# Performance work log

Measured on AMD Instinct MI355X. Metric: run time of the kernel, lower is better.

The kernel has to match this reference:

```python
import jax, jax.numpy as jnp
import numpy as np

D = 768; DEPTH = 12; NH = 12; DH = 64; MLP = 3072; P = 16; IMG = 224; HF = 14; FD = 256
B = 2; NV = 4


def _ln(x, g, b):
    m = x.mean(-1, keepdims=True)
    v = ((x - m) ** 2).mean(-1, keepdims=True)
    return (x - m) * jax.lax.rsqrt(v + 1e-6) * g + b


def _vit(x, patch_w, patch_b, cls_tok, pos_emb, blocks, nf_g, nf_b):
    # x: [n,3,224,224] -> tokens [n,197,768] (timm vit_base_patch16_224 forward_features)
    n = x.shape[0]
    p = x.reshape(n, 3, HF, P, HF, P).transpose(0, 2, 4, 1, 3, 5).reshape(n, HF * HF, 3 * P * P)
    tok = p @ patch_w + patch_b
    tok = jnp.concatenate([jnp.broadcast_to(cls_tok, (n, 1, D)), tok], axis=1) + pos_emb

    def block(t, pr):
        l1g, l1b, qw, qb, pw, pb, l2g, l2b, f1w, f1b, f2w, f2b = pr
        h = _ln(t, l1g, l1b)
        qkv = (h @ qw + qb).reshape(n, -1, 3, NH, DH)
        q, k, v = qkv[:, :, 0], qkv[:, :, 1], qkv[:, :, 2]
        att = jax.nn.softmax(jnp.einsum('bqhd,bkhd->bhqk', q, k) / jnp.sqrt(jnp.float32(DH)), axis=-1)
        o = jnp.einsum('bhqk,bkhd->bqhd', att, v).reshape(n, -1, D)
        t = t + o @ pw + pb
        h = _ln(t, l2g, l2b)
        t = t + jax.nn.gelu(h @ f1w + f1b, approximate=False) @ f2w + f2b
        return t, None

    tok, _ = jax.lax.scan(block, tok, blocks)
    return _ln(tok, nf_g, nf_b)


def setup_inputs() -> dict:
    key = jax.random.key(0)
    ks = jax.random.split(key, 24)
    s = 0.02
    imgs = jax.random.normal(ks[0], (B, NV, 3, IMG, IMG), jnp.float32)
    depths = jax.random.uniform(ks[1], (B, NV, IMG, IMG), jnp.float32) * 0.05  # scaled *65.535 -> (0,3.3), inside (0,5)
    t = jax.random.normal(ks[2], (B, NV, 3), jnp.float32) * 0.5
    poses = jnp.broadcast_to(jnp.eye(4, dtype=jnp.float32), (B, NV, 4, 4)).at[:, :, :3, 3].set(t)
    intr = (jnp.zeros((B, NV, 3, 3), jnp.float32)
            .at[:, :, 0, 0].set(200.0).at[:, :, 1, 1].set(200.0)
            .at[:, :, 0, 2].set(112.0).at[:, :, 1, 2].set(112.0).at[:, :, 2, 2].set(1.0))
    grid_points = jax.random.normal(ks[3], (B, 196, 3), jnp.float32)
    d = dict(
        ugv_images=imgs, ugv_depths=depths, camera_poses=poses, intrinsics=intr,
        grid_points_3d=grid_points,
        patch_w=jax.random.normal(ks[4], (3 * P * P, D), jnp.float32) * s,
        patch_b=jnp.zeros((D,), jnp.float32),
        cls_tok=jax.random.normal(ks[5], (1, 1, D), jnp.float32) * s,
        pos_emb=jax.random.normal(ks[6], (1, HF * HF + 1, D), jnp.float32) * s,
        ln1_g=jnp.ones((DEPTH, D), jnp.float32), ln1_b=jnp.zeros((DEPTH, D), jnp.float32),
        qkv_w=jax.random.normal(ks[7], (DEPTH, D, 3 * D), jnp.float32) * s,
        qkv_b=jnp.zeros((DEPTH, 3 * D), jnp.float32),
        proj_w=jax.random.normal(ks[8], (DEPTH, D, D), jnp.float32) * s,
        proj_b=jnp.zeros((DEPTH, D), jnp.float32),
        ln2_g=jnp.ones((DEPTH, D), jnp.float32), ln2_b=jnp.zeros((DEPTH, D), jnp.float32),
        fc1_w=jax.random.normal(ks[9], (DEPTH, D, MLP), jnp.float32) * s,
        fc1_b=jnp.zeros((DEPTH, MLP), jnp.float32),
        fc2_w=jax.random.normal(ks[10], (DEPTH, MLP, D), jnp.float32) * s,
        fc2_b=jnp.zeros((DEPTH, D), jnp.float32),
        nf_g=jnp.ones((D,), jnp.float32), nf_b=jnp.zeros((D,), jnp.float32),
        conv_w=jax.random.normal(ks[11], (FD, D), jnp.float32) * s,
        conv_b=jnp.zeros((FD,), jnp.float32),
    )
    return d


def reference(ugv_images, ugv_depths, camera_poses, intrinsics, grid_points_3d,
              patch_w, patch_b, cls_tok, pos_emb,
              ln1_g, ln1_b, qkv_w, qkv_b, proj_w, proj_b,
              ln2_g, ln2_b, fc1_w, fc1_b, fc2_w, fc2_b,
              nf_g, nf_b, conv_w, conv_b):
    blocks = (ln1_g, ln1_b, qkv_w, qkv_b, proj_w, proj_b, ln2_g, ln2_b, fc1_w, fc1_b, fc2_w, fc2_b)
    tok = _vit(ugv_images.reshape(B * NV, 3, IMG, IMG), patch_w, patch_b, cls_tok, pos_emb, blocks, nf_g, nf_b)
    feats = tok[:, 1:, :].transpose(0, 2, 1).reshape(B, NV, D, HF, HF)  # [B,N,C,Hf,Wf]

    # swap rows 0,1 of w2c, then invert
    w2c = camera_poses[:, :, jnp.array([1, 0, 2, 3]), :]
    c2w = jnp.linalg.inv(w2c)

    d = jax.image.resize(ugv_depths, (B, NV, HF, HF), 'linear', antialias=False) * (65535.0 / 1000.0)
    mask = (d > 0.0) & (d < 5.0)

    fx = intrinsics[:, :, 0, 0][..., None, None]
    fy = intrinsics[:, :, 1, 1][..., None, None]
    cx = intrinsics[:, :, 0, 2][..., None, None]
    cy = intrinsics[:, :, 1, 2][..., None, None]

    u, v = jnp.meshgrid(jnp.arange(HF, dtype=jnp.float32), jnp.arange(HF, dtype=jnp.float32), indexing='xy')
    Xc = -((u - cx) * d / (fx + 1e-8))
    Yc = (v - cy) * d / (fy + 1e-8)
    pts = jnp.stack([Xc, Yc, d, jnp.ones_like(d)], axis=-1)  # [B,N,Hf,Wf,4]
    w = jnp.einsum('bnij,bnhwj->bnhwi', c2w, pts)
    Xw, Yw = w[..., 0], w[..., 1]

    tile = 10.0
    px = Xw * (HF / tile) + HF / 2.0
    py = -(Yw * (HF / tile)) + HF / 2.0
    pxi = jnp.round(px).astype(jnp.int32)
    pyi = jnp.round(py).astype(jnp.int32)
    inb = (pxi >= 0) & (pxi < HF) & (pyi >= 0) & (pyi < HF)
    valid = mask & inb

    HW = HF * HF
    boff = jnp.arange(B, dtype=jnp.int32)[:, None, None, None] * HW
    idx = jnp.where(valid, boff + pyi * HF + pxi, B * HW).reshape(-1)  # invalid -> dummy bucket
    src = feats.transpose(0, 1, 3, 4, 2).reshape(-1, D)  # [B*N*HW, C]
    seg = B * HW + 1

    ssum = jax.ops.segment_sum(src, idx, num_segments=seg)
    cnt = jax.ops.segment_sum(valid.astype(jnp.float32).reshape(-1), idx, num_segments=seg)
    smax = jnp.zeros((seg, D), src.dtype).at[idx].max(src)  # include_self with 0 init, like torch amax

    avg = ssum[:B * HW] / (cnt[:B * HW, None] + 1e-8)
    bev = (avg + smax[:B * HW]) / 2.0
    bev = bev.reshape(B, HF, HF, D)
    out = jnp.einsum('bhwc,oc->bohw', bev, conv_w) + conv_b[None, :, None, None]
    return out
```

## Files before the change

### kernel.cpp

```cpp
#include <hip/hip_runtime.h>
#include <hip/hip_bf16.h>
#include <math.h>
#include <type_traits>
#include <utility>

#define DMODEL 768
#define NTOK 197
#define NIMG 8
#define NHEADS 12
#define MLPD 3072
#define NROWS (NIMG*NTOK)
#define NPATCH (NIMG*196)
#define HF 14
#define BATCH 2
#define NCELL (BATCH*HF*HF)
#define FD 256

typedef __attribute__((ext_vector_type(8))) short s8v;
typedef __attribute__((ext_vector_type(8))) __bf16 b8v;
typedef __attribute__((ext_vector_type(8))) _Float16 h8v;
typedef __attribute__((ext_vector_type(4))) float f32x4;

template <typename V, typename = void>
struct mfma_takes : std::false_type {};
template <typename V>
struct mfma_takes<V, std::void_t<decltype(
    __builtin_amdgcn_mfma_f32_16x16x32_bf16(std::declval<V>(), std::declval<V>(),
                                            std::declval<f32x4>(), 0, 0, 0))>>
    : std::true_type {};

template <typename V>
struct MfmaCall {
    static __device__ inline f32x4 run(s8v a, s8v b, f32x4 c) {
        return __builtin_amdgcn_mfma_f32_16x16x32_bf16(
            __builtin_bit_cast(V, a), __builtin_bit_cast(V, b), c, 0, 0, 0);
    }
};
using mfma_v = std::conditional_t<mfma_takes<b8v>::value, b8v, s8v>;

template <typename V, typename = void>
struct mfma16_takes : std::false_type {};
template <typename V>
struct mfma16_takes<V, std::void_t<decltype(
    __builtin_amdgcn_mfma_f32_16x16x32_f16(std::declval<V>(), std::declval<V>(),
                                           std::declval<f32x4>(), 0, 0, 0))>>
    : std::true_type {};

template <typename V>
struct MfmaF16Call {
    static __device__ inline f32x4 run(s8v a, s8v b, f32x4 c) {
        return __builtin_amdgcn_mfma_f32_16x16x32_f16(
            __builtin_bit_cast(V, a), __builtin_bit_cast(V, b), c, 0, 0, 0);
    }
};
using mfma16_v = std::conditional_t<mfma16_takes<h8v>::value, h8v, s8v>;

typedef __attribute__((address_space(1))) const unsigned int guint_t;
typedef __attribute__((address_space(3))) unsigned int luint_t;

template <int BM, int BN>
__global__ __launch_bounds__(256) void gemm_t(
    const __hip_bfloat16* __restrict__ A, const __hip_bfloat16* __restrict__ BT,
    const float* __restrict__ bias, const float* __restrict__ res,
    void* __restrict__ Cout, int M, int N, int K, int flags, int nx,
    float* __restrict__ part)
{
    constexpr int FM = BM / 32;
    constexpr int FN = BN / 32;
    __shared__ short Asl[BM * 32];
    __shared__ short Bsl[BN * 32];
    int t = threadIdx.x;
    int w = t >> 6, lane = t & 63;

    int nwg = gridDim.x;
    int id = blockIdx.x;
    int q = nwg >> 3, r = nwg & 7;
    int xcd = id & 7;
    int wgid = (xcd < r ? xcd * (q + 1) : r * (q + 1) + (xcd - r) * q) + (id >> 3);
    int bx = wgid % nx, by = wgid / nx;
    int bm = by * BM, bn = bx * BN;

    int S = gridDim.z, z = blockIdx.z;
    int kchunk = K / S;
    int kbeg = z * kchunk, kend = kbeg + kchunk;

    int rbase = (w >> 1) * (BM / 2), cbase = (w & 1) * (BN / 2);

    f32x4 acc[FM][FN];
    #pragma unroll
    for (int i = 0; i < FM; i++)
        #pragma unroll
        for (int j = 0; j < FN; j++)
            acc[i][j] = (f32x4){0.f, 0.f, 0.f, 0.f};

    const short* Ag = (const short*)A;
    const short* Bg = (const short*)BT;

    for (int k0 = kbeg; k0 < kend; k0 += 32) {
        #pragma unroll
        for (int i = 0; i < BM * 4 / 256; i++) {
            int c = i * 256 + t;
            int row = c >> 2, koff = (c & 3) * 8;
            int ga = bm + row; if (ga >= M) ga = M - 1;
            __builtin_amdgcn_global_load_lds(
                (guint_t*)(Ag + (size_t)ga * K + k0 + koff),
                (luint_t*)(Asl + c * 8), 16, 0, 0);
        }
        #pragma unroll
        for (int i = 0; i < BN * 4 / 256; i++) {
            int c = i * 256 + t;
            int row = c >> 2, koff = (c & 3) * 8;
            __builtin_amdgcn_global_load_lds(
                (guint_t*)(Bg + (size_t)(bn + row) * K + k0 + koff),
                (luint_t*)(Bsl + c * 8), 16, 0, 0);
        }
        __syncthreads();

        int kk = (lane >> 4) * 8;
        int rl = lane & 15;
        s8v af[FM], bfr[FN];
        #pragma unroll
        for (int i = 0; i < FM; i++)
            af[i] = *(const s8v*)(Asl + (rbase + i * 16 + rl) * 32 + kk);
        #pragma unroll
        for (int j = 0; j < FN; j++)
            bfr[j] = *(const s8v*)(Bsl + (cbase + j * 16 + rl) * 32 + kk);
        #pragma unroll
        for (int i = 0; i < FM; i++)
            #pragma unroll
            for (int j = 0; j < FN; j++)
                acc[i][j] = MfmaCall<mfma_v>::run(af[i], bfr[j], acc[i][j]);
        __syncthreads();
    }

    int colg = lane & 15;
    int rowg = (lane >> 4) * 4;
    #pragma unroll
    for (int i = 0; i < FM; i++) {
        #pragma unroll
        for (int j = 0; j < FN; j++) {
            #pragma unroll
            for (int qq = 0; qq < 4; qq++) {
                int rr = bm + rbase + i * 16 + rowg + qq;
                int cc = bn + cbase + j * 16 + colg;
                if (rr < M) {
                    float v = acc[i][j][qq];
                    if (flags & 8) {
                        part[((size_t)z * M + rr) * N + cc] = v;
                    } else {
                        if (bias) v += bias[cc];
                        if (flags & 1) v = 0.5f * v * (1.0f + erff(v * 0.7071067811865476f));
                        if (res)  v += res[(size_t)rr * N + cc];
                        if (flags & 2)
                            ((__hip_bfloat16*)Cout)[(size_t)rr * N + cc] = __float2bfloat16(v);
                        else if (flags & 4)
                            ((_Float16*)Cout)[(size_t)rr * N + cc] = (_Float16)v;
                        else
                            ((float*)Cout)[(size_t)rr * N + cc] = v;
                    }
                }
            }
        }
    }
}

__global__ __launch_bounds__(256) void fc2_reduce(
    const float* __restrict__ part, const float* __restrict__ bias,
    float* __restrict__ tok)
{
    int i = blockIdx.x * 256 + threadIdx.x;
    if (i >= NROWS * DMODEL / 4) return;
    float4 p0 = ((const float4*)part)[i];
    float4 p1 = ((const float4*)(part + (size_t)NROWS * DMODEL))[i];
    float4 tv = ((float4*)tok)[i];
    int c = (i * 4) % DMODEL;
    float4 bv = *(const float4*)(bias + c);
    tv.x += p0.x + p1.x + bv.x;
    tv.y += p0.y + p1.y + bv.y;
    tv.z += p0.z + p1.z + bv.z;
    tv.w += p0.w + p1.w + bv.w;
    ((float4*)tok)[i] = tv;
}

#define AT_STR 232
#define KS_STR 72

__global__ __launch_bounds__(256) void fused_attn_kernel(
    const _Float16* __restrict__ qkv, __hip_bfloat16* __restrict__ O)
{
    __shared__ char smem[29696 + 59392];
    _Float16* Vt = (_Float16*)smem;
    _Float16* Qs = (_Float16*)(smem + 29696);
    _Float16* Ks = Qs + 128 * KS_STR;
    _Float16* Pl = (_Float16*)(smem + 29696);

    int nh = blockIdx.x;
    int n = nh / NHEADS, hh = nh % NHEADS;
    int qoff = blockIdx.y * 128;
    int t = threadIdx.x;
    int w = t >> 6, lane = t & 63;
    int g = lane >> 4, rl = lane & 15;
    const _Float16* base = qkv + (size_t)n * NTOK * 2304;

    for (int idx = t; idx < 208 * 8; idx += 256) {
        int row = idx >> 3, c8 = (idx & 7) * 8;
        if (row < NTOK)
            *(uint4*)(Ks + row * KS_STR + c8) =
                *(const uint4*)(base + (size_t)row * 2304 + 768 + hh * 64 + c8);
        else
            *(uint4*)(Ks + row * KS_STR + c8) = make_uint4(0, 0, 0, 0);
    }
    for (int idx = t; idx < 128 * 8; idx += 256) {
        int row = idx >> 3, c8 = (idx & 7) * 8;
        int gq = qoff + row; if (gq > NTOK - 1) gq = NTOK - 1;
        *(uint4*)(Qs + row * KS_STR + c8) =
            *(const uint4*)(base + (size_t)gq * 2304 + hh * 64 + c8);
    }
    for (int idx = t; idx < NTOK * 8; idx += 256) {
        int k = idx >> 3, dg = (idx & 7) * 8;
        _Float16 tmp[8];
        *(uint4*)tmp = *(const uint4*)(base + (size_t)k * 2304 + 1536 + hh * 64 + dg);
        #pragma unroll
        for (int j = 0; j < 8; j++) Vt[(dg + j) * AT_STR + k] = tmp[j];
    }
    for (int idx = t; idx < 64 * 27; idx += 256) {
        int d = idx / 27, k = NTOK + idx % 27;
        Vt[d * AT_STR + k] = (_Float16)0.f;
    }
    __syncthreads();

    int wq0 = w * 32;
    f32x4 sacc[2][13];
    #pragma unroll
    for (int i = 0; i < 2; i++)
        #pragma unroll
        for (int tt = 0; tt < 13; tt++)
            sacc[i][tt] = (f32x4){0.f, 0.f, 0.f, 0.f};

    #pragma unroll
    for (int s = 0; s < 2; s++) {
        s8v af[2];
        #pragma unroll
        for (int i = 0; i < 2; i++)
            af[i] = *(const s8v*)(Qs + (wq0 + i * 16 + rl) * KS_STR + s * 32 + 8 * g);
        #pragma unroll
        for (int tt = 0; tt < 13; tt++) {
            s8v bf = *(const s8v*)(Ks + (tt * 16 + rl) * KS_STR + s * 32 + 8 * g);
            #pragma unroll
            for (int i = 0; i < 2; i++)
                sacc[i][tt] = MfmaF16Call<mfma16_v>::run(af[i], bf, sacc[i][tt]);
        }
    }
    __syncthreads();

    _Float16* Pw = Pl + w * 32 * AT_STR;
    #pragma unroll
    for (int i = 0; i < 2; i++) {
        #pragma unroll
        for (int r = 0; r < 4; r++) {
            float vv[13];
            float mx = -3.0e38f;
            #pragma unroll
            for (int tt = 0; tt < 13; tt++) {
                float v = sacc[i][tt][r] * 0.125f;
                vv[tt] = v;
                if (rl + 16 * tt < NTOK) mx = fmaxf(mx, v);
            }
            mx = fmaxf(mx, __shfl_xor(mx, 1));
            mx = fmaxf(mx, __shfl_xor(mx, 2));
            mx = fmaxf(mx, __shfl_xor(mx, 4));
            mx = fmaxf(mx, __shfl_xor(mx, 8));
            float pv[13];
            float sum = 0.f;
            #pragma unroll
            for (int tt = 0; tt < 13; tt++) {
                float p = (rl + 16 * tt < NTOK) ? __expf(vv[tt] - mx) : 0.f;
                pv[tt] = p; sum += p;
            }
            sum += __shfl_xor(sum, 1);
            sum += __shfl_xor(sum, 2);
            sum += __shfl_xor(sum, 4);
            sum += __shfl_xor(sum, 8);
            float rinv = 1.0f / sum;
            int prow = i * 16 + g * 4 + r;
            #pragma unroll
            for (int tt = 0; tt < 13; tt++)
                Pw[prow * AT_STR + rl + 16 * tt] = (_Float16)(pv[tt] * rinv);
        }
    }
    for (int idx = lane; idx < 32 * 16; idx += 64) {
        int rr = idx >> 4, cc = 208 + (idx & 15);
        Pw[rr * AT_STR + cc] = (_Float16)0.f;
    }

    f32x4 oacc[2][4];
    #pragma unroll
    for (int i = 0; i < 2; i++)
        #pragma unroll
        for (int j = 0; j < 4; j++)
            oacc[i][j] = (f32x4){0.f, 0.f, 0.f, 0.f};

    for (int s = 0; s < 7; s++) {
        s8v pf[2], vf[4];
        #pragma unroll
        for (int i = 0; i < 2; i++)
            pf[i] = *(const s8v*)(Pw + (i * 16 + rl) * AT_STR + s * 32 + 8 * g);
        #pragma unroll
        for (int j = 0; j < 4; j++)
            vf[j] = *(const s8v*)(Vt + (j * 16 + rl) * AT_STR + s * 32 + 8 * g);
        #pragma unroll
        for (int i = 0; i < 2; i++)
            #pragma unroll
            for (int j = 0; j < 4; j++)
                oacc[i][j] = MfmaF16Call<mfma16_v>::run(pf[i], vf[j], oacc[i][j]);
    }

    #pragma unroll
    for (int i = 0; i < 2; i++) {
        #pragma unroll
        for (int j = 0; j < 4; j++) {
            #pragma unroll
            for (int r = 0; r < 4; r++) {
                int qidx = qoff + wq0 + i * 16 + g * 4 + r;
                if (qidx < NTOK) {
                    int d = j * 16 + rl;
                    O[((size_t)n * NTOK + qidx) * DMODEL + hh * 64 + d] =
                        __float2bfloat16(oacc[i][j][r]);
                }
            }
        }
    }
}

__device__ inline void transpose_tile(const float* __restrict__ src,
                                      __hip_bfloat16* __restrict__ dst,
                                      int K, int N, int b)
{
    __shared__ float tl[32][33];
    int nt = N >> 5;
    int n0 = (b % nt) * 32, k0 = (b / nt) * 32;
    int tx = threadIdx.x & 31, ty = threadIdx.x >> 5;
    #pragma unroll
    for (int i = 0; i < 4; i++)
        tl[ty + i * 8][tx] = src[(size_t)(k0 + ty + i * 8) * N + n0 + tx];
    __syncthreads();
    #pragma unroll
    for (int i = 0; i < 4; i++)
        dst[(size_t)(n0 + ty + i * 8) * K + k0 + tx] = __float2bfloat16(tl[tx][ty + i * 8]);
}

__global__ __launch_bounds__(256) void convT(const float* __restrict__ src,
                                             __hip_bfloat16* __restrict__ dst,
                                             int K, int N)
{
    transpose_tile(src, dst, K, N, blockIdx.x);
}

__global__ __launch_bounds__(256) void convT4(
    const float* __restrict__ s0, const float* __restrict__ s1,
    const float* __restrict__ s2, const float* __restrict__ s3,
    __hip_bfloat16* __restrict__ d0, __hip_bfloat16* __restrict__ d1,
    __hip_bfloat16* __restrict__ d2, __hip_bfloat16* __restrict__ d3)
{
    int b = blockIdx.x;
    const float* src; __hip_bfloat16* dst; int K, N;
    if (b < 1728)      {            src = s0; dst = d0; K = 768;  N = 2304; }
    else if (b < 2304) { b -= 1728; src = s1; dst = d1; K = 768;  N = 768;  }
    else if (b < 4608) { b -= 2304; src = s2; dst = d2; K = 768;  N = 3072; }
    else               { b -= 4608; src = s3; dst = d3; K = 3072; N = 768;  }
    transpose_tile(src, dst, K, N, b);
}

__global__ __launch_bounds__(256) void patch_extract_kernel(
    const float* __restrict__ img, __hip_bfloat16* __restrict__ Pm)
{
    size_t e = (size_t)blockIdx.x * 256 + threadIdx.x;
    if (e >= (size_t)NPATCH * DMODEL) return;
    int cidx = (int)(e % DMODEL);
    int r    = (int)(e / DMODEL);
    int n  = r / 196, s = r % 196;
    int hi = s / HF, wi = s % HF;
    int c  = cidx >> 8, py = (cidx >> 4) & 15, px = cidx & 15;
    Pm[e] = __float2bfloat16(
        img[(((size_t)n * 3 + c) * 224 + hi * 16 + py) * 224 + wi * 16 + px]);
}

__global__ __launch_bounds__(256) void assemble_tok_kernel(
    const float* __restrict__ tmp, const float* __restrict__ cls,
    const float* __restrict__ pos, float* __restrict__ tok)
{
    size_t e = (size_t)blockIdx.x * 256 + threadIdx.x;
    if (e >= (size_t)NROWS * DMODEL) return;
    int d = (int)(e % DMODEL);
    size_t rr = e / DMODEL;
    int n = (int)(rr / NTOK), r = (int)(rr % NTOK);
    float v = (r == 0) ? cls[d] : tmp[((size_t)n * 196 + r - 1) * DMODEL + d];
    tok[e] = v + pos[(size_t)r * DMODEL + d];
}

template <int OUT_BF16>
__global__ __launch_bounds__(256) void ln_kernel(
    const float* __restrict__ X, const float* __restrict__ g,
    const float* __restrict__ b, void* __restrict__ Yv)
{
    int r = blockIdx.x;
    int t = threadIdx.x;
    const float* x = X + (size_t)r * DMODEL;
    float v0 = x[t], v1 = x[t + 256], v2 = x[t + 512];
    __shared__ float red[8];
    float s = v0 + v1 + v2;
    #pragma unroll
    for (int m = 32; m >= 1; m >>= 1) s += __shfl_xor(s, m);
    int wid = t >> 6, lane = t & 63;
    if (lane == 0) red[wid] = s;
    __syncthreads();
    float mean = (red[0] + red[1] + red[2] + red[3]) * (1.0f / DMODEL);
    float d0 = v0 - mean, d1 = v1 - mean, d2 = v2 - mean;
    float q = d0 * d0 + d1 * d1 + d2 * d2;
    #pragma unroll
    for (int m = 32; m >= 1; m >>= 1) q += __shfl_xor(q, m);
    __syncthreads();
    if (lane == 0) red[4 + wid] = q;
    __syncthreads();
    float var = (red[4] + red[5] + red[6] + red[7]) * (1.0f / DMODEL);
    float rs = 1.0f / sqrtf(var + 1e-6f);
    float y0 = d0 * rs * g[t] + b[t];
    float y1 = d1 * rs * g[t + 256] + b[t + 256];
    float y2 = d2 * rs * g[t + 512] + b[t + 512];
    if (OUT_BF16) {
        __hip_bfloat16* y = (__hip_bfloat16*)Yv + (size_t)r * DMODEL;
        y[t] = __float2bfloat16(y0);
        y[t + 256] = __float2bfloat16(y1);
        y[t + 512] = __float2bfloat16(y2);
    } else {
        float* y = (float*)Yv + (size_t)r * DMODEL;
        y[t] = y0; y[t + 256] = y1; y[t + 512] = y2;
    }
}

__device__ void invert4(const float m[16], float out[16]) {
    float inv[16];
    inv[0] = m[5]*m[10]*m[15] - m[5]*m[11]*m[14] - m[9]*m[6]*m[15] + m[9]*m[7]*m[14] + m[13]*m[6]*m[11] - m[13]*m[7]*m[10];
    inv[4] = -m[4]*m[10]*m[15] + m[4]*m[11]*m[14] + m[8]*m[6]*m[15] - m[8]*m[7]*m[14] - m[12]*m[6]*m[11] + m[12]*m[7]*m[10];
    inv[8] = m[4]*m[9]*m[15] - m[4]*m[11]*m[13] - m[8]*m[5]*m[15] + m[8]*m[7]*m[13] + m[12]*m[5]*m[11] - m[12]*m[7]*m[9];
    inv[12] = -m[4]*m[9]*m[14] + m[4]*m[10]*m[13] + m[8]*m[5]*m[14] - m[8]*m[6]*m[13] - m[12]*m[5]*m[10] + m[12]*m[6]*m[9];
    inv[1] = -m[1]*m[10]*m[15] + m[1]*m[11]*m[14] + m[9]*m[2]*m[15] - m[9]*m[3]*m[14] - m[13]*m[2]*m[11] + m[13]*m[3]*m[10];
    inv[5] = m[0]*m[10]*m[15] - m[0]*m[11]*m[14] - m[8]*m[2]*m[15] + m[8]*m[3]*m[14] + m[12]*m[2]*m[11] - m[12]*m[3]*m[10];
    inv[9] = -m[0]*m[9]*m[15] + m[0]*m[11]*m[13] + m[8]*m[1]*m[15] - m[8]*m[3]*m[13] - m[12]*m[1]*m[11] + m[12]*m[3]*m[9];
    inv[13] = m[0]*m[9]*m[14] - m[0]*m[10]*m[13] - m[8]*m[1]*m[14] + m[8]*m[2]*m[13] + m[12]*m[1]*m[10] - m[12]*m[2]*m[9];
    inv[2] = m[1]*m[6]*m[15] - m[1]*m[7]*m[14] - m[5]*m[2]*m[15] + m[5]*m[3]*m[14] + m[13]*m[2]*m[7] - m[13]*m[3]*m[6];
    inv[6] = -m[0]*m[6]*m[15] + m[0]*m[7]*m[14] + m[4]*m[2]*m[15] - m[4]*m[3]*m[14] - m[12]*m[2]*m[7] + m[12]*m[3]*m[6];
    inv[10] = m[0]*m[5]*m[15] - m[0]*m[7]*m[13] - m[4]*m[1]*m[15] + m[4]*m[3]*m[13] + m[12]*m[1]*m[7] - m[12]*m[3]*m[5];
    inv[14] = -m[0]*m[5]*m[14] + m[0]*m[6]*m[13] + m[4]*m[1]*m[14] - m[4]*m[2]*m[13] - m[12]*m[1]*m[6] + m[12]*m[2]*m[5];
    inv[3] = -m[1]*m[6]*m[11] + m[1]*m[7]*m[10] + m[5]*m[2]*m[11] - m[5]*m[3]*m[10] - m[9]*m[2]*m[7] + m[9]*m[3]*m[6];
    inv[7] = m[0]*m[6]*m[11] - m[0]*m[7]*m[10] - m[4]*m[2]*m[11] + m[4]*m[3]*m[10] + m[8]*m[2]*m[7] - m[8]*m[3]*m[6];
    inv[11] = -m[0]*m[5]*m[11] + m[0]*m[7]*m[9] + m[4]*m[1]*m[11] - m[4]*m[3]*m[9] - m[8]*m[1]*m[7] + m[8]*m[3]*m[5];
    inv[15] = m[0]*m[5]*m[10] - m[0]*m[6]*m[9] - m[4]*m[1]*m[10] + m[4]*m[2]*m[9] + m[8]*m[1]*m[6] - m[8]*m[2]*m[5];
    float det = m[0]*inv[0] + m[1]*inv[4] + m[2]*inv[8] + m[3]*inv[12];
    det = 1.0f / det;
    for (int i = 0; i < 16; i++) out[i] = inv[i] * det;
}

__global__ __launch_bounds__(256) void bev_index_kernel(
    const float* __restrict__ depths, const float* __restrict__ poses,
    const float* __restrict__ intr, int* __restrict__ idxbuf)
{
    int bv = blockIdx.x;
    int b  = bv / 4;
    __shared__ float c2w[16];
    if (threadIdx.x == 0) {
        float w2c[16];
        const float* Pm = poses + bv * 16;
        const int perm[4] = {1, 0, 2, 3};
        for (int i = 0; i < 4; i++)
            for (int j = 0; j < 4; j++)
                w2c[i * 4 + j] = Pm[perm[i] * 4 + j];
        invert4(w2c, c2w);
    }
    __syncthreads();
    int t = threadIdx.x;
    if (t >= 196) return;
    int hh = t / HF, ww = t % HF;
    const float* dp = depths + (size_t)bv * 224 * 224;
    int r0 = hh * 16 + 7, c0 = ww * 16 + 7;
    float d = 0.25f * (dp[r0 * 224 + c0] + dp[r0 * 224 + c0 + 1] +
                       dp[(r0 + 1) * 224 + c0] + dp[(r0 + 1) * 224 + c0 + 1]);
    d *= 65.535f;
    bool mask = (d > 0.0f) && (d < 5.0f);
    float fx = intr[bv * 9 + 0], fy = intr[bv * 9 + 4];
    float cx = intr[bv * 9 + 2], cy = intr[bv * 9 + 5];
    float u = (float)ww, v = (float)hh;
    float Xc = -((u - cx) * d / (fx + 1e-8f));
    float Yc = (v - cy) * d / (fy + 1e-8f);
    float Xw = c2w[0] * Xc + c2w[1] * Yc + c2w[2] * d + c2w[3];
    float Yw = c2w[4] * Xc + c2w[5] * Yc + c2w[6] * d + c2w[7];
    float px = Xw * 1.4f + 7.0f;
    float py = -(Yw * 1.4f) + 7.0f;
    int pxi = (int)rintf(px);
    int pyi = (int)rintf(py);
    bool inb = (pxi >= 0) && (pxi < HF) && (pyi >= 0) && (pyi < HF);
    idxbuf[bv * 196 + t] = (mask && inb) ? (b * 196 + pyi * HF + pxi) : -1;
}

__global__ __launch_bounds__(256) void splat_kernel(
    const float* __restrict__ src, const int* __restrict__ idxbuf,
    float* __restrict__ ssum, float* __restrict__ smax, float* __restrict__ cnt)
{
    int r = blockIdx.x;
    int idx = idxbuf[r];
    if (idx < 0) return;
    int bv = r / 196, s = r % 196;
    const float* row = src + ((size_t)bv * NTOK + 1 + s) * DMODEL;
    int t = threadIdx.x;
    for (int d = t; d < DMODEL; d += 256) {
        float v = row[d];
        atomicAdd(&ssum[(size_t)idx * DMODEL + d], v);
        atomicMax((int*)(smax + (size_t)idx * DMODEL + d), __float_as_int(v));
    }
    if (t == 0) atomicAdd(&cnt[idx], 1.0f);
}

__global__ __launch_bounds__(256) void bev_conv_kernel(
    const float* __restrict__ ssum, const float* __restrict__ smax,
    const float* __restrict__ cnt, const float* __restrict__ convw,
    const float* __restrict__ convb, float* __restrict__ out)
{
    int cell = blockIdx.x;
    __shared__ float bev[DMODEL];
    int t = threadIdx.x;
    float c = cnt[cell];
    for (int d = t; d < DMODEL; d += 256)
        bev[d] = 0.5f * (ssum[(size_t)cell * DMODEL + d] / (c + 1e-8f) +
                         smax[(size_t)cell * DMODEL + d]);
    __syncthreads();
    float acc = convb[t];
    const float4* wr = (const float4*)(convw + (size_t)t * DMODEL);
    #pragma unroll 4
    for (int dc = 0; dc < DMODEL / 4; dc++) {
        float4 w4 = wr[dc];
        acc += bev[dc * 4 + 0] * w4.x + bev[dc * 4 + 1] * w4.y +
               bev[dc * 4 + 2] * w4.z + bev[dc * 4 + 3] * w4.w;
    }
    int b = cell / 196, s = cell % 196;
    out[((size_t)b * FD + t) * 196 + s] = acc;
}

extern "C" void kernel_launch(void* const* d_in, const int* in_sizes, int n_in,
                              void* d_out, int out_size, void* d_ws, size_t ws_size,
                              hipStream_t stream) {
    const float* imgs    = (const float*)d_in[0];
    const float* depths  = (const float*)d_in[1];
    const float* poses   = (const float*)d_in[2];
    const float* intr    = (const float*)d_in[3];
    const float* patch_w = (const float*)d_in[5];
    const float* patch_b = (const float*)d_in[6];
    const float* cls_tok = (const float*)d_in[7];
    const float* pos_emb = (const float*)d_in[8];
    const float* ln1_g   = (const float*)d_in[9];
    const float* ln1_b   = (const float*)d_in[10];
    const float* qkv_w   = (const float*)d_in[11];
    const float* qkv_b   = (const float*)d_in[12];
    const float* proj_w  = (const float*)d_in[13];
    const float* proj_b  = (const float*)d_in[14];
    const float* ln2_g   = (const float*)d_in[15];
    const float* ln2_b   = (const float*)d_in[16];
    const float* fc1_w   = (const float*)d_in[17];
    const float* fc1_b   = (const float*)d_in[18];
    const float* fc2_w   = (const float*)d_in[19];
    const float* fc2_b   = (const float*)d_in[20];
    const float* nf_g    = (const float*)d_in[21];
    const float* nf_b    = (const float*)d_in[22];
    const float* conv_w  = (const float*)d_in[23];
    const float* conv_b  = (const float*)d_in[24];
    float* out = (float*)d_out;
    float* ws  = (float*)d_ws;

    const size_t OFF_TOK  = 0;
    const size_t OFF_FB   = OFF_TOK + 1210368;
    const size_t OFF_PB   = OFF_FB  + 3631104;
    const size_t OFF_HB   = OFF_PB  + 3725664;
    const size_t OFF_WQ   = OFF_HB  + 605184;
    const size_t OFF_WP   = OFF_WQ  + 884736;
    const size_t OFF_WF1  = OFF_WP  + 294912;
    const size_t OFF_WF2  = OFF_WF1 + 1179648;
    const size_t OFF_SSUM = OFF_WF2 + 1179648;
    const size_t OFF_SMAX = OFF_SSUM + 301056;
    const size_t OFF_CNT  = OFF_SMAX + 301056;
    const size_t OFF_IDX  = OFF_CNT + 512;

    float* tok  = ws + OFF_TOK;
    float* fbig = ws + OFF_FB;
    float* pbuf = ws + OFF_PB;
    _Float16* qkv_h = (_Float16*)pbuf;
    __hip_bfloat16* hb  = (__hip_bfloat16*)(ws + OFF_HB);
    __hip_bfloat16* wq  = (__hip_bfloat16*)(ws + OFF_WQ);
    __hip_bfloat16* wp  = (__hip_bfloat16*)(ws + OFF_WP);
    __hip_bfloat16* wf1 = (__hip_bfloat16*)(ws + OFF_WF1);
    __hip_bfloat16* wf2 = (__hip_bfloat16*)(ws + OFF_WF2);
    float* ssum = ws + OFF_SSUM;
    float* smax = ws + OFF_SMAX;
    float* cnt  = ws + OFF_CNT;
    int*   idxb = (int*)(ws + OFF_IDX);

    const int MT = (NROWS + 63) / 64;
    const int MTP = (NPATCH + 63) / 64;

    convT<<<576, 256, 0, stream>>>(patch_w, wq, 768, 768);
    patch_extract_kernel<<<(NPATCH * DMODEL) / 256, 256, 0, stream>>>(imgs, hb);
    gemm_t<64, 64><<<dim3(12 * MTP, 1, 1), 256, 0, stream>>>(
        hb, wq, patch_b, nullptr, fbig, NPATCH, 768, 768, 0, 12, nullptr);
    assemble_tok_kernel<<<(NROWS * DMODEL) / 256, 256, 0, stream>>>(
        fbig, cls_tok, pos_emb, tok);

    for (int l = 0; l < 12; l++) {
        convT4<<<6912, 256, 0, stream>>>(
            qkv_w + (size_t)l * DMODEL * 2304, proj_w + (size_t)l * DMODEL * DMODEL,
            fc1_w + (size_t)l * DMODEL * MLPD, fc2_w + (size_t)l * MLPD * DMODEL,
            wq, wp, wf1, wf2);
        ln_kernel<1><<<NROWS, 256, 0, stream>>>(tok, ln1_g + l * DMODEL, ln1_b + l * DMODEL, hb);
        gemm_t<64, 128><<<dim3(18 * MT, 1, 1), 256, 0, stream>>>(
            hb, wq, qkv_b + (size_t)l * 2304, nullptr, qkv_h, NROWS, 2304, 768,
            4 , 18, nullptr);
        fused_attn_kernel<<<dim3(NIMG * NHEADS, 2), 256, 0, stream>>>(qkv_h, hb);
        gemm_t<64, 64><<<dim3(12 * MT, 1, 1), 256, 0, stream>>>(
            hb, wp, proj_b + (size_t)l * DMODEL, tok, tok, NROWS, 768, 768,
            0, 12, nullptr);
        ln_kernel<1><<<NROWS, 256, 0, stream>>>(tok, ln2_g + l * DMODEL, ln2_b + l * DMODEL, hb);
        gemm_t<64, 128><<<dim3(24 * MT, 1, 1), 256, 0, stream>>>(
            hb, wf1, fc1_b + (size_t)l * MLPD, nullptr, pbuf, NROWS, 3072, 768,
            3 , 24, nullptr);
        gemm_t<64, 64><<<dim3(12 * MT, 1, 2), 256, 0, stream>>>(
            (__hip_bfloat16*)pbuf, wf2, nullptr, nullptr, nullptr, NROWS, 768, 3072,
            8 , 12, fbig);
        fc2_reduce<<<(NROWS * DMODEL / 4 + 255) / 256, 256, 0, stream>>>(
            fbig, fc2_b + (size_t)l * DMODEL, tok);
    }

    ln_kernel<0><<<NROWS, 256, 0, stream>>>(tok, nf_g, nf_b, fbig);

    bev_index_kernel<<<NIMG, 256, 0, stream>>>(depths, poses, intr, idxb);
    hipMemsetAsync(ssum, 0, (2 * (size_t)NCELL * DMODEL + 512) * sizeof(float), stream);
    splat_kernel<<<NPATCH, 256, 0, stream>>>(fbig, idxb, ssum, smax, cnt);

    bev_conv_kernel<<<NCELL, 256, 0, stream>>>(ssum, smax, cnt, conv_w, conv_b, out);
}
```

Baseline: 1.736 ms.

## Fuse residual-reduce with LayerNorm, batch weight transposes, shrink attention query tile

Residual adds (proj and fc2 split-K partials plus bias) are fused with the following LayerNorm into one row kernel, and token assembly is fused with the first LN. This removes separate elementwise and LN passes over the token buffer. All layer weight transposes run in a single up-front launch into a larger workspace instead of one launch per layer. The attention kernel now uses 64-query tiles (one 16-row strip per wave) with four y-blocks instead of two, for more blocks and fewer registers per wave. The cost is a larger workspace and the proj GEMM now writing fp32 partials that are re-read by the reduce kernel.

```diff
diff --git a/kernel.cpp b/kernel.cpp
--- a/kernel.cpp
+++ b/kernel.cpp
@@ -164,22 +164,93 @@
     }
 }
 
-__global__ __launch_bounds__(256) void fc2_reduce(
+template <int NPART, int FINAL>
+__global__ __launch_bounds__(256) void redln_kernel(
     const float* __restrict__ part, const float* __restrict__ bias,
-    float* __restrict__ tok)
-{
-    int i = blockIdx.x * 256 + threadIdx.x;
-    if (i >= NROWS * DMODEL / 4) return;
-    float4 p0 = ((const float4*)part)[i];
-    float4 p1 = ((const float4*)(part + (size_t)NROWS * DMODEL))[i];
-    float4 tv = ((float4*)tok)[i];
-    int c = (i * 4) % DMODEL;
-    float4 bv = *(const float4*)(bias + c);
-    tv.x += p0.x + p1.x + bv.x;
-    tv.y += p0.y + p1.y + bv.y;
-    tv.z += p0.z + p1.z + bv.z;
-    tv.w += p0.w + p1.w + bv.w;
-    ((float4*)tok)[i] = tv;
+    float* __restrict__ tok, const float* __restrict__ g,
+    const float* __restrict__ b, __hip_bfloat16* __restrict__ hout,
+    float* __restrict__ fout)
+{
+    int r = blockIdx.x, t = threadIdx.x;
+    __shared__ float red[8];
+    float v[3];
+    #pragma unroll
+    for (int i = 0; i < 3; i++) {
+        int idx = t + i * 256;
+        float x = tok[(size_t)r * DMODEL + idx] + bias[idx];
+        x += part[(size_t)r * DMODEL + idx];
+        if (NPART == 2) x += part[((size_t)NROWS + r) * DMODEL + idx];
+        v[i] = x;
+        if (!FINAL) tok[(size_t)r * DMODEL + idx] = x;
+    }
+    float s = v[0] + v[1] + v[2];
+    #pragma unroll
+    for (int m = 32; m >= 1; m >>= 1) s += __shfl_xor(s, m);
+    int wid = t >> 6, lane = t & 63;
+    if (lane == 0) red[wid] = s;
+    __syncthreads();
+    float mean = (red[0] + red[1] + red[2] + red[3]) * (1.0f / DMODEL);
+    float d0 = v[0] - mean, d1 = v[1] - mean, d2 = v[2] - mean;
+    float qv = d0 * d0 + d1 * d1 + d2 * d2;
+    #pragma unroll
+    for (int m = 32; m >= 1; m >>= 1) qv += __shfl_xor(qv, m);
+    __syncthreads();
+    if (lane == 0) red[4 + wid] = qv;
+    __syncthreads();
+    float var = (red[4] + red[5] + red[6] + red[7]) * (1.0f / DMODEL);
+    float rs = 1.0f / sqrtf(var + 1e-6f);
+    float dd[3] = {d0, d1, d2};
+    #pragma unroll
+    for (int i = 0; i < 3; i++) {
+        int idx = t + i * 256;
+        float y = dd[i] * rs * g[idx] + b[idx];
+        if (FINAL) fout[(size_t)r * DMODEL + idx] = y;
+        else       hout[(size_t)r * DMODEL + idx] = __float2bfloat16(y);
+    }
+}
+
+__global__ __launch_bounds__(256) void assemble_ln_kernel(
+    const float* __restrict__ tmp, const float* __restrict__ cls,
+    const float* __restrict__ pos, const float* __restrict__ g,
+    const float* __restrict__ b, float* __restrict__ tok,
+    __hip_bfloat16* __restrict__ hout)
+{
+    int rr = blockIdx.x;
+    int n = rr / NTOK, r = rr % NTOK;
+    int t = threadIdx.x;
+    __shared__ float red[8];
+    float v[3];
+    #pragma unroll
+    for (int i = 0; i < 3; i++) {
+        int idx = t + i * 256;
+        float x = (r == 0) ? cls[idx]
+                           : tmp[((size_t)n * 196 + r - 1) * DMODEL + idx];
+        x += pos[(size_t)r * DMODEL + idx];
+        v[i] = x;
+        tok[(size_t)rr * DMODEL + idx] = x;
+    }
+    float s = v[0] + v[1] + v[2];
+    #pragma unroll
+    for (int m = 32; m >= 1; m >>= 1) s += __shfl_xor(s, m);
+    int wid = t >> 6, lane = t & 63;
+    if (lane == 0) red[wid] = s;
+    __syncthreads();
+    float mean = (red[0] + red[1] + red[2] + red[3]) * (1.0f / DMODEL);
+    float d0 = v[0] - mean, d1 = v[1] - mean, d2 = v[2] - mean;
+    float qv = d0 * d0 + d1 * d1 + d2 * d2;
+    #pragma unroll
+    for (int m = 32; m >= 1; m >>= 1) qv += __shfl_xor(qv, m);
+    __syncthreads();
+    if (lane == 0) red[4 + wid] = qv;
+    __syncthreads();
+    float var = (red[4] + red[5] + red[6] + red[7]) * (1.0f / DMODEL);
+    float rs = 1.0f / sqrtf(var + 1e-6f);
+    float dd[3] = {d0, d1, d2};
+    #pragma unroll
+    for (int i = 0; i < 3; i++) {
+        int idx = t + i * 256;
+        hout[(size_t)rr * DMODEL + idx] = __float2bfloat16(dd[i] * rs * g[idx] + b[idx]);
+    }
 }
 
 #define AT_STR 232
@@ -188,15 +259,15 @@
 __global__ __launch_bounds__(256) void fused_attn_kernel(
     const _Float16* __restrict__ qkv, __hip_bfloat16* __restrict__ O)
 {
-    __shared__ char smem[29696 + 59392];
+    __shared__ char smem[29696 + 39168];
     _Float16* Vt = (_Float16*)smem;
     _Float16* Qs = (_Float16*)(smem + 29696);
-    _Float16* Ks = Qs + 128 * KS_STR;
+    _Float16* Ks = Qs + 64 * KS_STR;
     _Float16* Pl = (_Float16*)(smem + 29696);
 
     int nh = blockIdx.x;
     int n = nh / NHEADS, hh = nh % NHEADS;
-    int qoff = blockIdx.y * 128;
+    int qoff = blockIdx.y * 64;
     int t = threadIdx.x;
     int w = t >> 6, lane = t & 63;
     int g = lane >> 4, rl = lane & 15;
@@ -210,7 +281,7 @@
         else
             *(uint4*)(Ks + row * KS_STR + c8) = make_uint4(0, 0, 0, 0);
     }
-    for (int idx = t; idx < 128 * 8; idx += 256) {
+    for (int idx = t; idx < 64 * 8; idx += 256) {
         int row = idx >> 3, c8 = (idx & 7) * 8;
         int gq = qoff + row; if (gq > NTOK - 1) gq = NTOK - 1;
         *(uint4*)(Qs + row * KS_STR + c8) =
@@ -229,104 +300,83 @@
     }
     __syncthreads();
 
-    int wq0 = w * 32;
-    f32x4 sacc[2][13];
-    #pragma unroll
-    for (int i = 0; i < 2; i++)
-        #pragma unroll
-        for (int tt = 0; tt < 13; tt++)
-            sacc[i][tt] = (f32x4){0.f, 0.f, 0.f, 0.f};
+    int wq0 = w * 16;
+    f32x4 sacc[13];
+    #pragma unroll
+    for (int tt = 0; tt < 13; tt++) sacc[tt] = (f32x4){0.f, 0.f, 0.f, 0.f};
 
     #pragma unroll
     for (int s = 0; s < 2; s++) {
-        s8v af[2];
-        #pragma unroll
-        for (int i = 0; i < 2; i++)
-            af[i] = *(const s8v*)(Qs + (wq0 + i * 16 + rl) * KS_STR + s * 32 + 8 * g);
+        s8v af = *(const s8v*)(Qs + (wq0 + rl) * KS_STR + s * 32 + 8 * g);
         #pragma unroll
         for (int tt = 0; tt < 13; tt++) {
             s8v bf = *(const s8v*)(Ks + (tt * 16 + rl) * KS_STR + s * 32 + 8 * g);
-            #pragma unroll
-            for (int i = 0; i < 2; i++)
-                sacc[i][tt] = MfmaF16Call<mfma16_v>::run(af[i], bf, sacc[i][tt]);
-        }
-    }
-    __syncthreads();
-
-    _Float16* Pw = Pl + w * 32 * AT_STR;
-    #pragma unroll
-    for (int i = 0; i < 2; i++) {
-        #pragma unroll
-        for (int r = 0; r < 4; r++) {
-            float vv[13];
-            float mx = -3.0e38f;
-            #pragma unroll
-            for (int tt = 0; tt < 13; tt++) {
-                float v = sacc[i][tt][r] * 0.125f;
-                vv[tt] = v;
-                if (rl + 16 * tt < NTOK) mx = fmaxf(mx, v);
-            }
-            mx = fmaxf(mx, __shfl_xor(mx, 1));
-            mx = fmaxf(mx, __shfl_xor(mx, 2));
-            mx = fmaxf(mx, __shfl_xor(mx, 4));
-            mx = fmaxf(mx, __shfl_xor(mx, 8));
-            float pv[13];
-            float sum = 0.f;
-            #pragma unroll
-            for (int tt = 0; tt < 13; tt++) {
-                float p = (rl + 16 * tt < NTOK) ? __expf(vv[tt] - mx) : 0.f;
-                pv[tt] = p; sum += p;
-            }
-            sum += __shfl_xor(sum, 1);
-            sum += __shfl_xor(sum, 2);
-            sum += __shfl_xor(sum, 4);
-            sum += __shfl_xor(sum, 8);
-            float rinv = 1.0f / sum;
-            int prow = i * 16 + g * 4 + r;
-            #pragma unroll
-            for (int tt = 0; tt < 13; tt++)
-                Pw[prow * AT_STR + rl + 16 * tt] = (_Float16)(pv[tt] * rinv);
-        }
-    }
-    for (int idx = lane; idx < 32 * 16; idx += 64) {
+            sacc[tt] = MfmaF16Call<mfma16_v>::run(af, bf, sacc[tt]);
+        }
+    }
+    __syncthreads();
+
+    _Float16* Pw = Pl + wq0 * AT_STR;
+    #pragma unroll
+    for (int r = 0; r < 4; r++) {
+        float vv[13];
+        float mx = -3.0e38f;
+        #pragma unroll
+        for (int tt = 0; tt < 13; tt++) {
+            float v = sacc[tt][r] * 0.125f;
+            vv[tt] = v;
+            if (rl + 16 * tt < NTOK) mx = fmaxf(mx, v);
+        }
+        mx = fmaxf(mx, __shfl_xor(mx, 1));
+        mx = fmaxf(mx, __shfl_xor(mx, 2));
+        mx = fmaxf(mx, __shfl_xor(mx, 4));
+        mx = fmaxf(mx, __shfl_xor(mx, 8));
+        float pv[13];
+        float sum = 0.f;
+        #pragma unroll
+        for (int tt = 0; tt < 13; tt++) {
+            float p = (rl + 16 * tt < NTOK) ? __expf(vv[tt] - mx) : 0.f;
+            pv[tt] = p; sum += p;
+        }
+        sum += __shfl_xor(sum, 1);
+        sum += __shfl_xor(sum, 2);
+        sum += __shfl_xor(sum, 4);
+        sum += __shfl_xor(sum, 8);
+        float rinv = 1.0f / sum;
+        int prow = g * 4 + r;
+        #pragma unroll
+        for (int tt = 0; tt < 13; tt++)
+            Pw[prow * AT_STR + rl + 16 * tt] = (_Float16)(pv[tt] * rinv);
+    }
+    for (int idx = lane; idx < 16 * 16; idx += 64) {
         int rr = idx >> 4, cc = 208 + (idx & 15);
         Pw[rr * AT_STR + cc] = (_Float16)0.f;
     }
 
-    f32x4 oacc[2][4];
-    #pragma unroll
-    for (int i = 0; i < 2; i++)
-        #pragma unroll
-        for (int j = 0; j < 4; j++)
-            oacc[i][j] = (f32x4){0.f, 0.f, 0.f, 0.f};
+    f32x4 oacc[4];
+    #pragma unroll
+    for (int j = 0; j < 4; j++) oacc[j] = (f32x4){0.f, 0.f, 0.f, 0.f};
 
     for (int s = 0; s < 7; s++) {
-        s8v pf[2], vf[4];
-        #pragma unroll
-        for (int i = 0; i < 2; i++)
-            pf[i] = *(const s8v*)(Pw + (i * 16 + rl) * AT_STR + s * 32 + 8 * g);
+        s8v pf = *(const s8v*)(Pw + rl * AT_STR + s * 32 + 8 * g);
+        s8v vf[4];
         #pragma unroll
         for (int j = 0; j < 4; j++)
             vf[j] = *(const s8v*)(Vt + (j * 16 + rl) * AT_STR + s * 32 + 8 * g);
         #pragma unroll
-        for (int i = 0; i < 2; i++)
-            #pragma unroll
-            for (int j = 0; j < 4; j++)
-                oacc[i][j] = MfmaF16Call<mfma16_v>::run(pf[i], vf[j], oacc[i][j]);
-    }
-
-    #pragma unroll
-    for (int i = 0; i < 2; i++) {
-        #pragma unroll
-        for (int j = 0; j < 4; j++) {
-            #pragma unroll
-            for (int r = 0; r < 4; r++) {
-                int qidx = qoff + wq0 + i * 16 + g * 4 + r;
-                if (qidx < NTOK) {
-                    int d = j * 16 + rl;
-                    O[((size_t)n * NTOK + qidx) * DMODEL + hh * 64 + d] =
-                        __float2bfloat16(oacc[i][j][r]);
-                }
+        for (int j = 0; j < 4; j++)
+            oacc[j] = MfmaF16Call<mfma16_v>::run(pf, vf[j], oacc[j]);
+    }
+
+    #pragma unroll
+    for (int j = 0; j < 4; j++) {
+        #pragma unroll
+        for (int r = 0; r < 4; r++) {
+            int qidx = qoff + wq0 + g * 4 + r;
+            if (qidx < NTOK) {
+                int d = j * 16 + rl;
+                O[((size_t)n * NTOK + qidx) * DMODEL + hh * 64 + d] =
+                    __float2bfloat16(oacc[j][r]);
             }
         }
     }
@@ -349,26 +399,25 @@
         dst[(size_t)(n0 + ty + i * 8) * K + k0 + tx] = __float2bfloat16(tl[tx][ty + i * 8]);
 }
 
-__global__ __launch_bounds__(256) void convT(const float* __restrict__ src,
-                                             __hip_bfloat16* __restrict__ dst,
-                                             int K, int N)
-{
-    transpose_tile(src, dst, K, N, blockIdx.x);
-}
-
-__global__ __launch_bounds__(256) void convT4(
-    const float* __restrict__ s0, const float* __restrict__ s1,
-    const float* __restrict__ s2, const float* __restrict__ s3,
-    __hip_bfloat16* __restrict__ d0, __hip_bfloat16* __restrict__ d1,
-    __hip_bfloat16* __restrict__ d2, __hip_bfloat16* __restrict__ d3)
+__global__ __launch_bounds__(256) void convT_all(
+    const float* __restrict__ qkv_w, const float* __restrict__ proj_w,
+    const float* __restrict__ fc1_w, const float* __restrict__ fc2_w,
+    const float* __restrict__ patch_w,
+    __hip_bfloat16* __restrict__ wbuf, __hip_bfloat16* __restrict__ patchT)
 {
     int b = blockIdx.x;
-    const float* src; __hip_bfloat16* dst; int K, N;
-    if (b < 1728)      {            src = s0; dst = d0; K = 768;  N = 2304; }
-    else if (b < 2304) { b -= 1728; src = s1; dst = d1; K = 768;  N = 768;  }
-    else if (b < 4608) { b -= 2304; src = s2; dst = d2; K = 768;  N = 3072; }
-    else               { b -= 4608; src = s3; dst = d3; K = 3072; N = 768;  }
-    transpose_tile(src, dst, K, N, b);
+    if (b < 82944) {
+        int layer = b / 6912, rem = b % 6912;
+        __hip_bfloat16* wl = wbuf + (size_t)layer * 7077888;
+        const float* src; __hip_bfloat16* dst; int K, N, tb;
+        if (rem < 1728)      { tb = rem;        src = qkv_w  + (size_t)layer * 768 * 2304; dst = wl;           K = 768;  N = 2304; }
+        else if (rem < 2304) { tb = rem - 1728; src = proj_w + (size_t)layer * 768 * 768;  dst = wl + 1769472; K = 768;  N = 768;  }
+        else if (rem < 4608) { tb = rem - 2304; src = fc1_w  + (size_t)layer * 768 * 3072; dst = wl + 2359296; K = 768;  N = 3072; }
+        else                 { tb = rem - 4608; src = fc2_w  + (size_t)layer * 3072 * 768; dst = wl + 4718592; K = 3072; N = 768;  }
+        transpose_tile(src, dst, K, N, tb);
+    } else {
+        transpose_tile(patch_w, patchT, 768, 768, b - 82944);
+    }
 }
 
 __global__ __launch_bounds__(256) void patch_extract_kernel(
@@ -383,59 +432,6 @@
     int c  = cidx >> 8, py = (cidx >> 4) & 15, px = cidx & 15;
     Pm[e] = __float2bfloat16(
         img[(((size_t)n * 3 + c) * 224 + hi * 16 + py) * 224 + wi * 16 + px]);
-}
-
-__global__ __launch_bounds__(256) void assemble_tok_kernel(
-    const float* __restrict__ tmp, const float* __restrict__ cls,
-    const float* __restrict__ pos, float* __restrict__ tok)
-{
-    size_t e = (size_t)blockIdx.x * 256 + threadIdx.x;
-    if (e >= (size_t)NROWS * DMODEL) return;
-    int d = (int)(e % DMODEL);
-    size_t rr = e / DMODEL;
-    int n = (int)(rr / NTOK), r = (int)(rr % NTOK);
-    float v = (r == 0) ? cls[d] : tmp[((size_t)n * 196 + r - 1) * DMODEL + d];
-    tok[e] = v + pos[(size_t)r * DMODEL + d];
-}
-
-template <int OUT_BF16>
-__global__ __launch_bounds__(256) void ln_kernel(
-    const float* __restrict__ X, const float* __restrict__ g,
-    const float* __restrict__ b, void* __restrict__ Yv)
-{
-    int r = blockIdx.x;
-    int t = threadIdx.x;
-    const float* x = X + (size_t)r * DMODEL;
-    float v0 = x[t], v1 = x[t + 256], v2 = x[t + 512];
-    __shared__ float red[8];
-    float s = v0 + v1 + v2;
-    #pragma unroll
-    for (int m = 32; m >= 1; m >>= 1) s += __shfl_xor(s, m);
-    int wid = t >> 6, lane = t & 63;
-    if (lane == 0) red[wid] = s;
-    __syncthreads();
-    float mean = (red[0] + red[1] + red[2] + red[3]) * (1.0f / DMODEL);
-    float d0 = v0 - mean, d1 = v1 - mean, d2 = v2 - mean;
-    float q = d0 * d0 + d1 * d1 + d2 * d2;
-    #pragma unroll
-    for (int m = 32; m >= 1; m >>= 1) q += __shfl_xor(q, m);
-    __syncthreads();
-    if (lane == 0) red[4 + wid] = q;
-    __syncthreads();
-    float var = (red[4] + red[5] + red[6] + red[7]) * (1.0f / DMODEL);
-    float rs = 1.0f / sqrtf(var + 1e-6f);
-    float y0 = d0 * rs * g[t] + b[t];
-    float y1 = d1 * rs * g[t + 256] + b[t + 256];
-    float y2 = d2 * rs * g[t + 512] + b[t + 512];
-    if (OUT_BF16) {
-        __hip_bfloat16* y = (__hip_bfloat16*)Yv + (size_t)r * DMODEL;
-        y[t] = __float2bfloat16(y0);
-        y[t + 256] = __float2bfloat16(y1);
-        y[t + 512] = __float2bfloat16(y2);
-    } else {
-        float* y = (float*)Yv + (size_t)r * DMODEL;
-        y[t] = y0; y[t + 256] = y1; y[t + 512] = y2;
-    }
 }
 
 __device__ void invert4(const float m[16], float out[16]) {
@@ -576,27 +572,23 @@
     float* ws  = (float*)d_ws;
 
     const size_t OFF_TOK  = 0;
-    const size_t OFF_FB   = OFF_TOK + 1210368;
-    const size_t OFF_PB   = OFF_FB  + 3631104;
-    const size_t OFF_HB   = OFF_PB  + 3725664;
-    const size_t OFF_WQ   = OFF_HB  + 605184;
-    const size_t OFF_WP   = OFF_WQ  + 884736;
-    const size_t OFF_WF1  = OFF_WP  + 294912;
-    const size_t OFF_WF2  = OFF_WF1 + 1179648;
-    const size_t OFF_SSUM = OFF_WF2 + 1179648;
-    const size_t OFF_SMAX = OFF_SSUM + 301056;
-    const size_t OFF_CNT  = OFF_SMAX + 301056;
-    const size_t OFF_IDX  = OFF_CNT + 512;
+    const size_t OFF_FB   = 1210368;
+    const size_t OFF_PB   = 3631104;
+    const size_t OFF_HB   = 6051840;
+    const size_t OFF_PT   = 6657024;
+    const size_t OFF_SSUM = 6951936;
+    const size_t OFF_SMAX = 7252992;
+    const size_t OFF_CNT  = 7554048;
+    const size_t OFF_IDX  = 7554560;
+    const size_t OFF_W    = 7556608;
 
     float* tok  = ws + OFF_TOK;
     float* fbig = ws + OFF_FB;
     float* pbuf = ws + OFF_PB;
     _Float16* qkv_h = (_Float16*)pbuf;
     __hip_bfloat16* hb  = (__hip_bfloat16*)(ws + OFF_HB);
-    __hip_bfloat16* wq  = (__hip_bfloat16*)(ws + OFF_WQ);
-    __hip_bfloat16* wp  = (__hip_bfloat16*)(ws + OFF_WP);
-    __hip_bfloat16* wf1 = (__hip_bfloat16*)(ws + OFF_WF1);
-    __hip_bfloat16* wf2 = (__hip_bfloat16*)(ws + OFF_WF2);
+    __hip_bfloat16* pT  = (__hip_bfloat16*)(ws + OFF_PT);
+    __hip_bfloat16* wbuf = (__hip_bfloat16*)(ws + OFF_W);
     float* ssum = ws + OFF_SSUM;
     float* smax = ws + OFF_SMAX;
     float* cnt  = ws + OFF_CNT;
@@ -605,42 +597,51 @@
     const int MT = (NROWS + 63) / 64;
     const int MTP = (NPATCH + 63) / 64;
 
-    convT<<<576, 256, 0, stream>>>(patch_w, wq, 768, 768);
+    convT_all<<<83520, 256, 0, stream>>>(qkv_w, proj_w, fc1_w, fc2_w, patch_w, wbuf, pT);
+
     patch_extract_kernel<<<(NPATCH * DMODEL) / 256, 256, 0, stream>>>(imgs, hb);
     gemm_t<64, 64><<<dim3(12 * MTP, 1, 1), 256, 0, stream>>>(
-        hb, wq, patch_b, nullptr, fbig, NPATCH, 768, 768, 0, 12, nullptr);
-    assemble_tok_kernel<<<(NROWS * DMODEL) / 256, 256, 0, stream>>>(
-        fbig, cls_tok, pos_emb, tok);
+        hb, pT, patch_b, nullptr, fbig, NPATCH, 768, 768, 0, 12, nullptr);
+    assemble_ln_kernel<<<NROWS, 256, 0, stream>>>(
+        fbig, cls_tok, pos_emb, ln1_g, ln1_b, tok, hb);
 
     for (int l = 0; l < 12; l++) {
-        convT4<<<6912, 256, 0, stream>>>(
-            qkv_w + (size_t)l * DMODEL * 2304, proj_w + (size_t)l * DMODEL * DMODEL,
-            fc1_w + (size_t)l * DMODEL * MLPD, fc2_w + (size_t)l * MLPD * DMODEL,
-            wq, wp, wf1, wf2);
-        ln_kernel<1><<<NROWS, 256, 0, stream>>>(tok, ln1_g + l * DMODEL, ln1_b + l * DMODEL, hb);
+        __hip_bfloat16* wl  = wbuf + (size_t)l * 7077888;
+        __hip_bfloat16* wq  = wl;
+        __hip_bfloat16* wp  = wl + 1769472;
+        __hip_bfloat16* wf1 = wl + 2359296;
+        __hip_bfloat16* wf2 = wl + 4718592;
+
         gemm_t<64, 128><<<dim3(18 * MT, 1, 1), 256, 0, stream>>>(
             hb, wq, qkv_b + (size_t)l * 2304, nullptr, qkv_h, NROWS, 2304, 768,
             4 , 18, nullptr);
-        fused_attn_kernel<<<dim3(NIMG * NHEADS, 2), 256, 0, stream>>>(qkv_h, hb);
+        fused_attn_kernel<<<dim3(NIMG * NHEADS, 4), 256, 0, stream>>>(qkv_h, hb);
         gemm_t<64, 64><<<dim3(12 * MT, 1, 1), 256, 0, stream>>>(
-            hb, wp, proj_b + (size_t)l * DMODEL, tok, tok, NROWS, 768, 768,
-            0, 12, nullptr);
-        ln_kernel<1><<<NROWS, 256, 0, stream>>>(tok, ln2_g + l * DMODEL, ln2_b + l * DMODEL, hb);
+            hb, wp, nullptr, nullptr, nullptr, NROWS, 768, 768,
+            8 , 12, fbig);
+        redln_kernel<1, 0><<<NROWS, 256, 0, stream>>>(
+            fbig, proj_b + (size_t)l * DMODEL, tok,
+            ln2_g + l * DMODEL, ln2_b + l * DMODEL, hb, nullptr);
         gemm_t<64, 128><<<dim3(24 * MT, 1, 1), 256, 0, stream>>>(
             hb, wf1, fc1_b + (size_t)l * MLPD, nullptr, pbuf, NROWS, 3072, 768,
             3 , 24, nullptr);
         gemm_t<64, 64><<<dim3(12 * MT, 1, 2), 256, 0, stream>>>(
             (__hip_bfloat16*)pbuf, wf2, nullptr, nullptr, nullptr, NROWS, 768, 3072,
             8 , 12, fbig);
-        fc2_reduce<<<(NROWS * DMODEL / 4 + 255) / 256, 256, 0, stream>>>(
-            fbig, fc2_b + (size_t)l * DMODEL, tok);
-    }
-
-    ln_kernel<0><<<NROWS, 256, 0, stream>>>(tok, nf_g, nf_b, fbig);
+        if (l < 11) {
+            redln_kernel<2, 0><<<NROWS, 256, 0, stream>>>(
+                fbig, fc2_b + (size_t)l * DMODEL, tok,
+                ln1_g + (l + 1) * DMODEL, ln1_b + (l + 1) * DMODEL, hb, nullptr);
+        } else {
+            redln_kernel<2, 1><<<NROWS, 256, 0, stream>>>(
+                fbig, fc2_b + (size_t)l * DMODEL, tok,
+                nf_g, nf_b, nullptr, pbuf);
+        }
+    }
 
     bev_index_kernel<<<NIMG, 256, 0, stream>>>(depths, poses, intr, idxb);
     hipMemsetAsync(ssum, 0, (2 * (size_t)NCELL * DMODEL + 512) * sizeof(float), stream);
-    splat_kernel<<<NPATCH, 256, 0, stream>>>(fbig, idxb, ssum, smax, cnt);
+    splat_kernel<<<NPATCH, 256, 0, stream>>>(pbuf, idxb, ssum, smax, cnt);
 
     bev_conv_kernel<<<NCELL, 256, 0, stream>>>(ssum, smax, cnt, conv_w, conv_b, out);
 }
```

Result: faster. 1.681 ms (-3.2%).
